# Performance work log

Measured on AMD Instinct MI355X. Metric: run time of the kernel, lower is better.

## Reference

```python
import jax, jax.numpy as jnp
import numpy as np

NEIGHBOUR_NUM = 8  # args.neighbour_num


def _sqrdis_map(x, y):
    # x: [B,M,3], y: [B,N,3] -> [B,M,N] squared distances
    x2 = jnp.sum(x * x, axis=-1)
    y2 = jnp.sum(y * y, axis=-1)
    inner = jnp.einsum('bmd,bnd->bmn', x, y)
    return x2[:, :, None] + y2[:, None, :] - 2.0 * inner


def _chamfer(x, y):
    d = _sqrdis_map(x, y)
    return d.min(axis=2), d.min(axis=1)


def _neighbor_index(v, k):
    # torch.topk(dist, k+1, largest=False) then drop self
    d = _sqrdis_map(v, v)
    idx = jax.lax.top_k(-d, k + 1)[1]  # ascending distance order
    return idx[:, :, 1:]


def _arap(idx, dp, sp):
    B = dp.shape[0]
    bid = jnp.arange(B)[:, None, None]
    dn = dp[bid, idx] - dp[:, :, None, :]  # [B,N,K,3]
    sn = sp[bid, idx] - sp[:, :, None, :]
    dd = jnp.sqrt(jnp.sum(dn * dn, axis=-1) + 1e-5)
    sd = jnp.sqrt(jnp.sum(sn * sn, axis=-1) + 1e-5)
    diff = dd - sd
    return jnp.sum(diff * diff) / B


def setup_inputs() -> dict:
    key = jax.random.key(0)
    ks = jax.random.split(key, 7)
    T, B, N = 3, 4, 4096
    return {
        'phi': jax.random.normal(ks[0], (T, B, 1024), dtype=jnp.float32),
        'point_weight': jax.random.normal(ks[1], (T, B, N, 1), dtype=jnp.float32),
        'deform_rigid_points': 0.5 * jax.random.normal(ks[2], (T, B, N, 3), dtype=jnp.float32),
        'deformation_points': 0.5 * jax.random.normal(ks[3], (T, B, N, 3), dtype=jnp.float32),
        'rigid_matrix': 0.1 * jax.random.normal(ks[4], (T, B, 4, 4), dtype=jnp.float32),
        'source_points': jax.random.uniform(ks[5], (B, N, 3), dtype=jnp.float32, minval=-1.0, maxval=1.0),
        'target_points': jax.random.uniform(ks[6], (B, N, 3), dtype=jnp.float32, minval=-1.0, maxval=1.0),
    }


def reference(phi, point_weight, deform_rigid_points, deformation_points,
              rigid_matrix, source_points, target_points):
    B = source_points.shape[0]
    T = phi.shape[0]  # iter_time = len(phi_list)
    idx = _neighbor_index(source_points, NEIGHBOUR_NUM)
    trans_mask = jnp.zeros((4, 4), dtype=rigid_matrix.dtype).at[0:3, 3].set(1.0)
    total = jnp.asarray(0.0, dtype=source_points.dtype)
    for t in range(T):  # small fixed iter count, structurally distinct stages
        dp = deformation_points[t]
        # loss_on_cd
        d1, d2 = _chamfer(dp, target_points)
        cd = (jnp.sum(d1) + jnp.sum(d2)) * 0.5 / B
        # loss_on_pd (rigid-deformed vs full deformation)
        diff = deform_rigid_points[t] - dp
        pd = jnp.sum(diff * diff) / B
        # loss_on_sparse
        sp = jnp.mean(jnp.abs(point_weight[t]))
        # loss_on_tran
        tr = trans_mask[None] * rigid_matrix[t]
        tran = jnp.sum(tr * tr) / B
        # loss_on_arap
        ar = _arap(idx, dp, source_points)
        total = total + cd + pd + sp + tran + ar
    return total
```

## Files before the change

### kernel.cpp

```cpp
#include <hip/hip_runtime.h>

#define T_ 3
#define B_ 4
#define N_ 4096
#define K_ 8

#define KNN_BLOCKS (B_ * (N_ / 16))
#define CH_BLOCKS  (T_ * B_ * 2 * 16)
#define KWIN 1024
#define CWIN 512

typedef short bf16x8 __attribute__((ext_vector_type(8)));
typedef float f32x4  __attribute__((ext_vector_type(4)));

template <int NW>
__device__ inline float block_reduce(float v, float* scratch) {
    #pragma unroll
    for (int off = 32; off > 0; off >>= 1) v += __shfl_down(v, off, 64);
    const int lane = threadIdx.x & 63, wid = threadIdx.x >> 6;
    if (lane == 0) scratch[wid] = v;
    __syncthreads();
    float s = 0.f;
    if (threadIdx.x == 0) {
        #pragma unroll
        for (int w = 0; w < NW; ++w) s += scratch[w];
    }
    return s;
}

#define CE_(A, i, j) { unsigned lo_ = min(A[i], A[j]); A[j] = max(A[i], A[j]); A[i] = lo_; }
__device__ inline void sort8(unsigned s[8]) {
    CE_(s,0,1) CE_(s,2,3) CE_(s,4,5) CE_(s,6,7)
    CE_(s,0,2) CE_(s,1,3) CE_(s,4,6) CE_(s,5,7)
    CE_(s,1,2) CE_(s,5,6)
    CE_(s,0,4) CE_(s,1,5) CE_(s,2,6) CE_(s,3,7)
    CE_(s,2,4) CE_(s,3,5)
    CE_(s,1,2) CE_(s,3,4) CE_(s,5,6)
}
__device__ inline void merge_top8(unsigned a[8], const unsigned s[8]) {
    #pragma unroll
    for (int i = 0; i < 8; ++i) a[i] = min(a[i], s[7 - i]);
    CE_(a,0,4) CE_(a,1,5) CE_(a,2,6) CE_(a,3,7)
    CE_(a,0,2) CE_(a,1,3) CE_(a,4,6) CE_(a,5,7)
    CE_(a,0,1) CE_(a,2,3) CE_(a,4,5) CE_(a,6,7)
}

__device__ inline short hi16(float v) { return (short)(__float_as_uint(v) >> 16); }
__device__ inline float residual(float v) {
    return v - __uint_as_float(__float_as_uint(v) & 0xFFFF0000u);
}
__device__ inline unsigned pk2(short a, short b) {
    return (unsigned)(unsigned short)a | ((unsigned)(unsigned short)b << 16);
}
#define BF16_ONE ((short)0x3F80)

__global__ __launch_bounds__(256, 4) void mega_kernel(const float* __restrict__ src,
                                                      const float* __restrict__ dp_all,
                                                      const float* __restrict__ tp,
                                                      int* __restrict__ idx,
                                                      float* __restrict__ out) {
    __shared__ uint4 smem4[1088];

    if (blockIdx.x < KNN_BLOCKS) {
        float4* win = (float4*)smem4;
        const int b  = blockIdx.x / (N_ / 16);
        const int q0 = (blockIdx.x % (N_ / 16)) * 16;
        const float* sb = src + (size_t)b * N_ * 3;

        const int qp = threadIdx.x >> 5;
        const int c  = threadIdx.x & 31;
        const int i0 = q0 + 2 * qp, i1 = i0 + 1;
        const float qx0 = sb[3 * i0], qy0 = sb[3 * i0 + 1], qz0 = sb[3 * i0 + 2];
        const float qx1 = sb[3 * i1], qy1 = sb[3 * i1 + 1], qz1 = sb[3 * i1 + 2];
        const float q20 = fmaf(qx0, qx0, fmaf(qy0, qy0, qz0 * qz0));
        const float q21 = fmaf(qx1, qx1, fmaf(qy1, qy1, qz1 * qz1));

        unsigned a0[K_], a1[K_];
        #pragma unroll
        for (int p = 0; p < K_; ++p) { a0[p] = 0xFFFFFFFFu; a1[p] = 0xFFFFFFFFu; }

        for (int w = 0; w < N_ / KWIN; ++w) {
            __syncthreads();
            for (int j = threadIdx.x; j < KWIN; j += 256) {
                int jg = w * KWIN + j;
                float x = sb[3 * jg], y = sb[3 * jg + 1], z = sb[3 * jg + 2];
                win[j] = make_float4(-2.f * x, -2.f * y, -2.f * z,
                                     fmaf(x, x, fmaf(y, y, z * z)));
            }
            __syncthreads();

            #pragma unroll
            for (int bt = 0; bt < KWIN / 8 / 32; ++bt) {
                unsigned s0[8], s1[8];
                #pragma unroll
                for (int u = 0; u < 8; ++u) {
                    int jl = 32 * (bt * 8 + u) + c;
                    float4 cd = win[jl];
                    int jglob = w * KWIN + jl;
                    float d0 = fmaf(qx0, cd.x, fmaf(qy0, cd.y, fmaf(qz0, cd.z, cd.w))) + q20;
                    float d1 = fmaf(qx1, cd.x, fmaf(qy1, cd.y, fmaf(qz1, cd.z, cd.w))) + q21;
                    unsigned p0 = (__float_as_uint(d0) & 0xFFFFF000u) | (unsigned)jglob;
                    unsigned p1 = (__float_as_uint(d1) & 0xFFFFF000u) | (unsigned)jglob;
                    s0[u] = (jglob == i0) ? 0xFFFFFFFFu : p0;
                    s1[u] = (jglob == i1) ? 0xFFFFFFFFu : p1;
                }
                sort8(s0); merge_top8(a0, s0);
                sort8(s1); merge_top8(a1, s1);
            }
        }
        __syncthreads();

        unsigned* sm = (unsigned*)smem4;
        for (int half = 16; half >= 1; half >>= 1) {
            #pragma unroll
            for (int e = 0; e < K_; ++e) {
                sm[(e * 32 + c) * 17 + 2 * qp]     = a0[e];
                sm[(e * 32 + c) * 17 + 2 * qp + 1] = a1[e];
            }
            __syncthreads();
            if (c < half) {
                unsigned t0[8], t1[8];
                #pragma unroll
                for (int e = 0; e < K_; ++e) {
                    t0[e] = sm[(e * 32 + c + half) * 17 + 2 * qp];
                    t1[e] = sm[(e * 32 + c + half) * 17 + 2 * qp + 1];
                }
                merge_top8(a0, t0);
                merge_top8(a1, t1);
            }
            __syncthreads();
        }

        if (c == 0) {
            int* op0 = idx + ((size_t)b * N_ + i0) * K_;
            int* op1 = idx + ((size_t)b * N_ + i1) * K_;
            #pragma unroll
            for (int k = 0; k < K_; ++k) {
                op0[k] = (int)(a0[k] & 0xFFFu);
                op1[k] = (int)(a1[k] & 0xFFFu);
            }
        }
    } else {
        uint4* alds = smem4;
        const int cb   = blockIdx.x - KNN_BLOCKS;
        const int tbd  = cb >> 4;
        const int slab = cb & 15;
        const int dir = tbd & 1;
        const int tb  = tbd >> 1;
        const int b = tb % B_, t = tb / B_;

        const float* dpb = dp_all + ((size_t)(t * B_ + b)) * N_ * 3;
        const float* tpb = tp + (size_t)b * N_ * 3;
        const float* cbase = dir ? dpb : tpb;
        const float* qbase = dir ? tpb : dpb;

        const int lane = threadIdx.x & 63;
        const int wave = threadIdx.x >> 6;
        const int quad = lane >> 4;
        const int n    = lane & 15;

        bf16x8 bfrag[4];
        float  q2r[4];
        #pragma unroll
        for (int s = 0; s < 4; ++s) {
            int qid = slab * 256 + wave * 64 + s * 16 + n;
            float x = qbase[3 * qid], y = qbase[3 * qid + 1], z = qbase[3 * qid + 2];
            q2r[s] = fmaf(x, x, fmaf(y, y, z * z));
            short hx = hi16(x), hy = hi16(y), hz = hi16(z);
            short lx = hi16(residual(x)), ly = hi16(residual(y)), lz = hi16(residual(z));
            if (quad == 0)
                bfrag[s] = (bf16x8){hx, hy, hz, hx, hy, hz, BF16_ONE, BF16_ONE};
            else if (quad == 1)
                bfrag[s] = (bf16x8){lx, ly, lz, lx, ly, lz, 0, 0};
            else
                bfrag[s] = (bf16x8)(short)0;
        }

        float run[4] = {3.4e38f, 3.4e38f, 3.4e38f, 3.4e38f};
        const f32x4 zero4 = {0.f, 0.f, 0.f, 0.f};

        for (int w = 0; w < N_ / CWIN; ++w) {
            __syncthreads();
            #pragma unroll
            for (int r = 0; r < 2; ++r) {
                int jloc = threadIdx.x * 2 + r;
                int jg = w * CWIN + jloc;
                float x = cbase[3 * jg], y = cbase[3 * jg + 1], z = cbase[3 * jg + 2];
                float p2 = fmaf(x, x, fmaf(y, y, z * z));
                float mx = -2.f * x, my = -2.f * y, mz = -2.f * z;
                short mhx = hi16(mx), mhy = hi16(my), mhz = hi16(mz);
                short mlx = hi16(residual(mx)), mly = hi16(residual(my)), mlz = hi16(residual(mz));
                short p2h = hi16(p2), p2l = hi16(residual(p2));
                uint4 f0 = make_uint4(pk2(mhx, mhy), pk2(mhz, mlx), pk2(mly, mlz), pk2(p2h, p2l));
                uint4 f1 = make_uint4(f0.x, f0.y, f0.z, 0u);
                int tile = jloc >> 4, m = jloc & 15;
                alds[tile * 32 + m]      = f0;
                alds[tile * 32 + 16 + m] = f1;
            }
            __syncthreads();

            #pragma unroll 4
            for (int tile = 0; tile < CWIN / 16; ++tile) {
                bf16x8 af = (bf16x8)(short)0;
                if (quad < 2) {
                    union { uint4 u; bf16x8 v; } cv;
                    cv.u = alds[tile * 32 + quad * 16 + n];
                    af = cv.v;
                }
                #pragma unroll
                for (int s = 0; s < 4; ++s) {
                    f32x4 d = __builtin_amdgcn_mfma_f32_16x16x32_bf16(af, bfrag[s], zero4, 0, 0, 0);
                    float r3 = fminf(fminf(d[0], d[1]), d[2]);
                    run[s] = fminf(fminf(run[s], r3), d[3]);
                }
            }
        }

        float vsum = 0.f;
        #pragma unroll
        for (int s = 0; s < 4; ++s) {
            float r = run[s];
            r = fminf(r, __shfl_xor(r, 32));
            r = fminf(r, __shfl_xor(r, 16));
            if (lane < 16) vsum += r + q2r[s];
        }
        __syncthreads();
        float ssum = block_reduce<4>(vsum, (float*)smem4);
        if (threadIdx.x == 0) atomicAdd(out, ssum * (0.5f / B_));
    }
}

__global__ __launch_bounds__(256) void finalize_kernel(const float* __restrict__ dp_all,
                                                       const float* __restrict__ src,
                                                       const int* __restrict__ idx,
                                                       const float* __restrict__ drp,
                                                       const float* __restrict__ pw,
                                                       const float* __restrict__ rm,
                                                       float* __restrict__ out) {
    __shared__ float red[4];
    const int blk = blockIdx.x;

    if (blk < 192) {
        const int chunk = blk & 15;
        const int tb = blk >> 4;
        const int b = tb % B_, t = tb / B_;
        const int n = chunk * 256 + threadIdx.x;
        const float* dp = dp_all + ((size_t)t * B_ + b) * (N_ * 3);
        const float* sp = src + (size_t)b * (N_ * 3);
        const float px = dp[n * 3], py = dp[n * 3 + 1], pz = dp[n * 3 + 2];
        const float sx = sp[n * 3], sy = sp[n * 3 + 1], sz = sp[n * 3 + 2];
        const int* ip = idx + ((size_t)b * N_ + n) * K_;
        float acc = 0.f;
        #pragma unroll
        for (int k = 0; k < K_; ++k) {
            int j = ip[k];
            float dx = dp[j * 3] - px, dy = dp[j * 3 + 1] - py, dz = dp[j * 3 + 2] - pz;
            float ex = sp[j * 3] - sx, ey = sp[j * 3 + 1] - sy, ez = sp[j * 3 + 2] - sz;
            float dd = sqrtf(fmaf(dx, dx, fmaf(dy, dy, dz * dz)) + 1e-5f);
            float sd = sqrtf(fmaf(ex, ex, fmaf(ey, ey, ez * ez)) + 1e-5f);
            float df = dd - sd;
            acc = fmaf(df, df, acc);
        }
        float s = block_reduce<4>(acc, red);
        if (threadIdx.x == 0) atomicAdd(out, s * (1.0f / B_));
    } else {
        const int PD_N = T_ * B_ * N_ * 3;
        const int SP_N = T_ * B_ * N_;
        const int stride = 32 * 256;
        const int gid = (blk - 192) * 256 + threadIdx.x;
        float apd = 0.f;
        for (int i = gid; i < PD_N; i += stride) {
            float d = drp[i] - dp_all[i];
            apd = fmaf(d, d, apd);
        }
        float asp = 0.f;
        for (int i = gid; i < SP_N; i += stride) asp += fabsf(pw[i]);
        float atr = 0.f;
        if (gid < T_ * B_ * 3) {
            int t = gid / (B_ * 3);
            int b = (gid / 3) % B_;
            int r = gid % 3;
            float v = rm[t * B_ * 16 + b * 16 + r * 4 + 3];
            atr = v * v;
        }
        float acc = apd * (1.0f / B_) + asp * (1.0f / (B_ * N_)) + atr * (1.0f / B_);
        float s = block_reduce<4>(acc, red);
        if (threadIdx.x == 0) atomicAdd(out, s);
    }
}

extern "C" void kernel_launch(void* const* d_in, const int* in_sizes, int n_in,
                              void* d_out, int out_size, void* d_ws, size_t ws_size,
                              hipStream_t stream) {
    const float* pw  = (const float*)d_in[1];
    const float* drp = (const float*)d_in[2];
    const float* dp  = (const float*)d_in[3];
    const float* rm  = (const float*)d_in[4];
    const float* sp  = (const float*)d_in[5];
    const float* tp  = (const float*)d_in[6];
    float* out = (float*)d_out;

    int* idx = (int*)d_ws;

    hipMemsetAsync(out, 0, sizeof(float), stream);
    mega_kernel<<<KNN_BLOCKS + CH_BLOCKS, 256, 0, stream>>>(sp, dp, tp, idx, out);
    finalize_kernel<<<224, 256, 0, stream>>>(dp, sp, idx, drp, pw, rm, out);
}
```

Measured before the change: 133.2 us.

## Fuse ARAP loss and small losses into mega kernel, drop finalize launch

```diff
diff --git a/kernel.cpp b/kernel.cpp
--- a/kernel.cpp
+++ b/kernel.cpp
@@ -7,6 +7,7 @@
 
 #define KNN_BLOCKS (B_ * (N_ / 16))
 #define CH_BLOCKS  (T_ * B_ * 2 * 16)
+#define SL_BLOCKS  32
 #define KWIN 1024
 #define CWIN 512
 
@@ -54,10 +55,12 @@
 }
 #define BF16_ONE ((short)0x3F80)
 
-__global__ __launch_bounds__(256, 4) void mega_kernel(const float* __restrict__ src,
+__global__ __launch_bounds__(256, 6) void mega_kernel(const float* __restrict__ src,
                                                       const float* __restrict__ dp_all,
                                                       const float* __restrict__ tp,
-                                                      int* __restrict__ idx,
+                                                      const float* __restrict__ drp,
+                                                      const float* __restrict__ pw,
+                                                      const float* __restrict__ rm,
                                                       float* __restrict__ out) {
     __shared__ uint4 smem4[1088];
 
@@ -131,16 +134,40 @@
             __syncthreads();
         }
 
+        unsigned* nidx = (unsigned*)smem4 + 64;
         if (c == 0) {
-            int* op0 = idx + ((size_t)b * N_ + i0) * K_;
-            int* op1 = idx + ((size_t)b * N_ + i1) * K_;
-            #pragma unroll
-            for (int k = 0; k < K_; ++k) {
-                op0[k] = (int)(a0[k] & 0xFFFu);
-                op1[k] = (int)(a1[k] & 0xFFFu);
-            }
-        }
-    } else {
+            #pragma unroll
+            for (int e = 0; e < K_; ++e) {
+                nidx[(2 * qp) * K_ + e]     = a0[e] & 0xFFFu;
+                nidx[(2 * qp + 1) * K_ + e] = a1[e] & 0xFFFu;
+            }
+        }
+        __syncthreads();
+
+        float acc = 0.f;
+        if (threadIdx.x < 16 * K_) {
+            const int q  = threadIdx.x >> 3;
+            const int qi = q0 + q;
+            const int j  = (int)nidx[threadIdx.x];
+            float sx = sb[3 * qi], sy = sb[3 * qi + 1], sz = sb[3 * qi + 2];
+            float ex = sb[3 * j] - sx, ey = sb[3 * j + 1] - sy, ez = sb[3 * j + 2] - sz;
+            float sd = sqrtf(fmaf(ex, ex, fmaf(ey, ey, ez * ez)) + 1e-5f);
+            #pragma unroll
+            for (int t = 0; t < T_; ++t) {
+                const float* dpb = dp_all + ((size_t)(t * B_ + b)) * N_ * 3;
+                float dx = dpb[3 * j] - dpb[3 * qi];
+                float dy = dpb[3 * j + 1] - dpb[3 * qi + 1];
+                float dz = dpb[3 * j + 2] - dpb[3 * qi + 2];
+                float dd = sqrtf(fmaf(dx, dx, fmaf(dy, dy, dz * dz)) + 1e-5f);
+                float df = dd - sd;
+                acc = fmaf(df, df, acc);
+            }
+        }
+        __syncthreads();
+        float s = block_reduce<4>(acc, (float*)smem4);
+        if (threadIdx.x == 0) atomicAdd(out, s * (1.0f / B_));
+
+    } else if (blockIdx.x < KNN_BLOCKS + CH_BLOCKS) {
         uint4* alds = smem4;
         const int cb   = blockIdx.x - KNN_BLOCKS;
         const int tbd  = cb >> 4;
@@ -227,47 +254,12 @@
         __syncthreads();
         float ssum = block_reduce<4>(vsum, (float*)smem4);
         if (threadIdx.x == 0) atomicAdd(out, ssum * (0.5f / B_));
-    }
-}
-
-__global__ __launch_bounds__(256) void finalize_kernel(const float* __restrict__ dp_all,
-                                                       const float* __restrict__ src,
-                                                       const int* __restrict__ idx,
-                                                       const float* __restrict__ drp,
-                                                       const float* __restrict__ pw,
-                                                       const float* __restrict__ rm,
-                                                       float* __restrict__ out) {
-    __shared__ float red[4];
-    const int blk = blockIdx.x;
-
-    if (blk < 192) {
-        const int chunk = blk & 15;
-        const int tb = blk >> 4;
-        const int b = tb % B_, t = tb / B_;
-        const int n = chunk * 256 + threadIdx.x;
-        const float* dp = dp_all + ((size_t)t * B_ + b) * (N_ * 3);
-        const float* sp = src + (size_t)b * (N_ * 3);
-        const float px = dp[n * 3], py = dp[n * 3 + 1], pz = dp[n * 3 + 2];
-        const float sx = sp[n * 3], sy = sp[n * 3 + 1], sz = sp[n * 3 + 2];
-        const int* ip = idx + ((size_t)b * N_ + n) * K_;
-        float acc = 0.f;
-        #pragma unroll
-        for (int k = 0; k < K_; ++k) {
-            int j = ip[k];
-            float dx = dp[j * 3] - px, dy = dp[j * 3 + 1] - py, dz = dp[j * 3 + 2] - pz;
-            float ex = sp[j * 3] - sx, ey = sp[j * 3 + 1] - sy, ez = sp[j * 3 + 2] - sz;
-            float dd = sqrtf(fmaf(dx, dx, fmaf(dy, dy, dz * dz)) + 1e-5f);
-            float sd = sqrtf(fmaf(ex, ex, fmaf(ey, ey, ez * ez)) + 1e-5f);
-            float df = dd - sd;
-            acc = fmaf(df, df, acc);
-        }
-        float s = block_reduce<4>(acc, red);
-        if (threadIdx.x == 0) atomicAdd(out, s * (1.0f / B_));
+
     } else {
         const int PD_N = T_ * B_ * N_ * 3;
         const int SP_N = T_ * B_ * N_;
-        const int stride = 32 * 256;
-        const int gid = (blk - 192) * 256 + threadIdx.x;
+        const int stride = SL_BLOCKS * 256;
+        const int gid = (blockIdx.x - KNN_BLOCKS - CH_BLOCKS) * 256 + threadIdx.x;
         float apd = 0.f;
         for (int i = gid; i < PD_N; i += stride) {
             float d = drp[i] - dp_all[i];
@@ -284,7 +276,7 @@
             atr = v * v;
         }
         float acc = apd * (1.0f / B_) + asp * (1.0f / (B_ * N_)) + atr * (1.0f / B_);
-        float s = block_reduce<4>(acc, red);
+        float s = block_reduce<4>(acc, (float*)smem4);
         if (threadIdx.x == 0) atomicAdd(out, s);
     }
 }
@@ -300,9 +292,7 @@
     const float* tp  = (const float*)d_in[6];
     float* out = (float*)d_out;
 
-    int* idx = (int*)d_ws;
-
     hipMemsetAsync(out, 0, sizeof(float), stream);
-    mega_kernel<<<KNN_BLOCKS + CH_BLOCKS, 256, 0, stream>>>(sp, dp, tp, idx, out);
-    finalize_kernel<<<224, 256, 0, stream>>>(dp, sp, idx, drp, pw, rm, out);
-}
+    mega_kernel<<<KNN_BLOCKS + CH_BLOCKS + SL_BLOCKS, 256, 0, stream>>>(
+        sp, dp, tp, drp, pw, rm, out);
+}
```

Result: faster. 126.5 us (-5.0%).
